# Kernel optimization log

Hardware: AMD Instinct MI355X
Metric: run time of the kernel (lower is better)

The kernel has to match this reference:

```python
import jax, jax.numpy as jnp
import numpy as np

N, NF, INF, NHID = 8192, 128, 128, 16


def _gcn(x, adj, dis, W, b):
    # GraphConvolution: support = x @ W; aggregate with distance-weighted adjacency
    support = x @ W  # [N, out]
    return (adj * dis) @ support + b


def setup_inputs() -> dict:
    key = jax.random.key(0)
    ks = jax.random.split(key, 26)

    def lin(k, i, o):
        kw, kb = jax.random.split(k)
        W = jax.random.uniform(kw, (i, o), jnp.float32, -1.0, 1.0) / np.sqrt(i).astype(np.float32)
        b = jax.random.uniform(kb, (o,), jnp.float32, -1.0, 1.0) / np.sqrt(i).astype(np.float32)
        return W, b

    x = jax.random.normal(ks[0], (N, NF), jnp.float32)
    adj = jax.random.uniform(ks[1], (N, N), jnp.float32)
    dis = jax.random.uniform(ks[2], (N, N), jnp.float32)

    W1, b1 = lin(ks[3], NF, NF)        # linear1
    Wg1, bg1 = lin(ks[4], NF, INF)     # gc1
    Wm1, bm1 = lin(ks[5], INF, 64)     # linear_med1
    Wm2, bm2 = lin(ks[6], 64, 128)     # linear_med2
    Wm3, bm3 = lin(ks[7], 128, 64)     # linear_med3
    Wm4, bm4 = lin(ks[8], 64, 64)      # linear_med4
    Wgh, bgh = lin(ks[9], 64, 64)      # gconv_hidden[0]
    W2, b2 = lin(ks[10], 64, 32)       # linear2
    Wg2, bg2 = lin(ks[11], 32, 32)     # gc2
    W3, b3 = lin(ks[12], 32, NHID)     # linear3

    return dict(x=x, adj=adj, dis=dis, W1=W1, b1=b1, Wg1=Wg1, bg1=bg1,
                Wm1=Wm1, bm1=bm1, Wm2=Wm2, bm2=bm2, Wm3=Wm3, bm3=bm3,
                Wm4=Wm4, bm4=bm4, Wgh=Wgh, bgh=bgh, W2=W2, b2=b2,
                Wg2=Wg2, bg2=bg2, W3=W3, b3=b3)


def reference(x, adj, dis, W1, b1, Wg1, bg1, Wm1, bm1, Wm2, bm2, Wm3, bm3,
              Wm4, bm4, Wgh, bgh, W2, b2, Wg2, bg2, W3, b3):
    lrelu = lambda v: jax.nn.leaky_relu(v, 0.2)
    x0 = _gcn(x @ W1 + b1, adj, dis, Wg1, bg1)
    x0 = lrelu(x0 @ Wm1 + bm1)
    x0 = lrelu(x0 @ Wm2 + bm2)
    x0 = lrelu(x0 @ Wm3 + bm3)
    x0 = jax.nn.relu(x0 @ Wm4 + bm4)
    x_res = x0
    x0 = jax.nn.relu(_gcn(x0, adj, dis, Wgh, bgh) + x_res)  # one hidden gconv layer
    x0 = x0 @ W2 + b2
    x0 = _gcn(x0, adj, dis, Wg2, bg2)
    return x0 @ W3 + b3
```

## Files before the change

kernel.cpp:

```cpp
#include <hip/hip_runtime.h>
#include <hip/hip_bf16.h>

#define NROWS 8192
typedef unsigned short u16;
typedef short bf16x8 __attribute__((ext_vector_type(8)));
typedef short bf16x4 __attribute__((ext_vector_type(4)));
typedef float f32x4 __attribute__((ext_vector_type(4)));

__device__ __forceinline__ u16 f2b(float f) {
    unsigned u = __float_as_uint(f);
    unsigned r = (u + 0x7fffu + ((u >> 16) & 1u)) >> 16;
    return (u16)r;
}
__device__ __forceinline__ float b2f(u16 v) {
    return __uint_as_float(((unsigned)v) << 16);
}

template<int MODE> __device__ __forceinline__ float actf(float v) {
    if constexpr (MODE == 1) return fmaxf(v, 0.f);
    else if constexpr (MODE == 2) return v > 0.f ? v : 0.2f * v;
    else return v;
}

__global__ __launch_bounds__(256) void fold1(
    const float* __restrict__ W1, const float* __restrict__ b1,
    const float* __restrict__ Wg1,
    const float* __restrict__ W2, const float* __restrict__ b2,
    const float* __restrict__ Wg2, float* __restrict__ ws) {
    float* T2 = ws + 9376;
    float* v1 = ws + 11424;
    float* v2 = ws + 11552;
    float* T1 = ws + 16384;
    const int tid = threadIdx.x, b = blockIdx.x;
    if (b < 16) {
        int i = b * 8 + (tid >> 5), j4 = (tid & 31) << 2;
        float4 acc = {0, 0, 0, 0};
        for (int k = 0; k < 128; ++k) {
            float a = W1[i * 128 + k];
            float4 g = *(const float4*)&Wg1[k * 128 + j4];
            acc.x += a * g.x; acc.y += a * g.y; acc.z += a * g.z; acc.w += a * g.w;
        }
        *(float4*)&T1[i * 128 + j4] = acc;
    } else if (b == 16) {
        if (tid < 128) {
            float s = 0;
            for (int k = 0; k < 128; ++k) s += b1[k] * Wg1[k * 128 + tid];
            v1[tid] = s;
        } else if (tid < 160) {
            int j = tid - 128;
            float s = 0;
            for (int k = 0; k < 32; ++k) s += b2[k] * Wg2[k * 32 + j];
            v2[j] = s;
        }
    } else {
        for (int o4 = tid; o4 < 64 * 8; o4 += 256) {
            int i = o4 >> 3, j4 = (o4 & 7) << 2;
            float4 acc = {0, 0, 0, 0};
            for (int k = 0; k < 32; ++k) {
                float a = W2[i * 32 + k];
                float4 g = *(const float4*)&Wg2[k * 32 + j4];
                acc.x += a * g.x; acc.y += a * g.y; acc.z += a * g.z; acc.w += a * g.w;
            }
            *(float4*)&T2[i * 32 + j4] = acc;
        }
    }
}

__global__ __launch_bounds__(256) void fold2(
    const float* __restrict__ Wm1, const float* __restrict__ bm1,
    const float* __restrict__ bg1,
    const float* __restrict__ W3, const float* __restrict__ b3,
    const float* __restrict__ bg2, float* __restrict__ ws) {
    float* WA = ws + 0;
    float* bA = ws + 8192;
    float* cA = ws + 8256;
    float* WB = ws + 8320;
    float* bB = ws + 9344;
    float* cB = ws + 9360;
    const float* T2 = ws + 9376;
    const float* v1 = ws + 11424;
    const float* v2 = ws + 11552;
    const float* T1 = ws + 16384;
    const int tid = threadIdx.x, b = blockIdx.x;
    if (b < 8) {
        int i = b * 16 + (tid >> 4), j4 = (tid & 15) << 2;
        float4 acc = {0, 0, 0, 0};
        for (int k = 0; k < 128; ++k) {
            float a = T1[i * 128 + k];
            float4 g = *(const float4*)&Wm1[k * 64 + j4];
            acc.x += a * g.x; acc.y += a * g.y; acc.z += a * g.z; acc.w += a * g.w;
        }
        *(float4*)&WA[i * 64 + j4] = acc;
    } else if (b == 8) {
        if (tid < 64) {
            float s = 0, c = 0;
            for (int k = 0; k < 128; ++k) {
                s += v1[k] * Wm1[k * 64 + tid];
                c += bg1[k] * Wm1[k * 64 + tid];
            }
            bA[tid] = s; cA[tid] = c + bm1[tid];
        } else if (tid < 80) {
            int j = tid - 64;
            float s = 0, c = 0;
            for (int k = 0; k < 32; ++k) {
                s += v2[k] * W3[k * 16 + j];
                c += bg2[k] * W3[k * 16 + j];
            }
            bB[j] = s; cB[j] = c + b3[j];
        }
    } else {
        int i = tid >> 2, j4 = (tid & 3) << 2;
        float4 acc = {0, 0, 0, 0};
        for (int k = 0; k < 32; ++k) {
            float a = T2[i * 32 + k];
            float4 g = *(const float4*)&W3[k * 16 + j4];
            acc.x += a * g.x; acc.y += a * g.y; acc.z += a * g.z; acc.w += a * g.w;
        }
        *(float4*)&WB[i * 16 + j4] = acc;
    }
}

template<int K, int M, int AIN, int AOUT, int OUTT>
__global__ __launch_bounds__(256) void gemm_rows(
    const float* __restrict__ in, const float* __restrict__ W,
    const float* __restrict__ bias, void* __restrict__ outv) {
    constexpr int RB = 32;
    constexpr int TNs = (M >= 64) ? 4 : 2;
    constexpr int TXs = M / TNs;
    constexpr int TYs = 256 / TXs;
    constexpr int TMs = RB / TYs;
    static_assert(TMs >= 1 && TMs * TYs == RB, "bad cfg");
    __shared__ float in_t[K][RB + 4];
    __shared__ float w_s[K * M];
    __shared__ float bias_s[M];
    const int tid = threadIdx.x;
    const int b0 = blockIdx.x * RB;
    constexpr int K4 = K / 4;
    for (int g = tid; g < RB * K4; g += 256) {
        int r = g / K4, c4 = g % K4;
        float4 v = *(const float4*)&in[(size_t)(b0 + r) * K + c4 * 4];
        v.x = actf<AIN>(v.x); v.y = actf<AIN>(v.y);
        v.z = actf<AIN>(v.z); v.w = actf<AIN>(v.w);
        in_t[c4 * 4 + 0][r] = v.x;
        in_t[c4 * 4 + 1][r] = v.y;
        in_t[c4 * 4 + 2][r] = v.z;
        in_t[c4 * 4 + 3][r] = v.w;
    }
    for (int g = tid; g < K * M / 4; g += 256)
        ((float4*)w_s)[g] = ((const float4*)W)[g];
    if (tid < M) bias_s[tid] = bias ? bias[tid] : 0.f;
    __syncthreads();

    const int tx = tid % TXs, ty = tid / TXs;
    const int c0 = tx * TNs, r0 = ty * TMs;
    float acc[TMs][TNs] = {};
    for (int k = 0; k < K; ++k) {
        float a[TMs];
#pragma unroll
        for (int m = 0; m < TMs; ++m) a[m] = in_t[k][r0 + m];
        float w[TNs];
#pragma unroll
        for (int n = 0; n < TNs; ++n) w[n] = w_s[k * M + c0 + n];
#pragma unroll
        for (int m = 0; m < TMs; ++m)
#pragma unroll
            for (int n = 0; n < TNs; ++n) acc[m][n] += a[m] * w[n];
    }
#pragma unroll
    for (int m = 0; m < TMs; ++m) {
        float vres[TNs];
#pragma unroll
        for (int n = 0; n < TNs; ++n) vres[n] = actf<AOUT>(acc[m][n] + bias_s[c0 + n]);
        if constexpr (OUTT == 0) {
            float* op = &((float*)outv)[(size_t)(b0 + r0 + m) * M + c0];
            if constexpr (TNs == 4) { float4 o4 = {vres[0], vres[1], vres[2], vres[3]}; *(float4*)op = o4; }
            else                    { float2 o2 = {vres[0], vres[1]}; *(float2*)op = o2; }
        } else {
            u16* ot = (u16*)outv;
#pragma unroll
            for (int n = 0; n < TNs; ++n)
                ot[(size_t)(c0 + n) * NROWS + (b0 + r0 + m)] = f2b(vres[n]);
        }
    }
}

template<int K, int M, int AOUT, int OMODE>
__device__ __forceinline__ void layer_step(
    const float (*pin)[17], const float* __restrict__ w,
    const float* __restrict__ bias,
    float (*pout)[17], float* __restrict__ gout, u16* __restrict__ stout,
    int b0, int tid) {
    constexpr int TXs = M / 4;
    constexpr int TYs = 256 / TXs;
    constexpr int TMs = 16 / TYs;
    static_assert(TMs >= 1, "cfg");
    const int tx = tid % TXs, ty = tid / TXs;
    const int c0 = tx * 4, r0 = ty * TMs;
    float acc[TMs][4] = {};
    for (int k = 0; k < K; ++k) {
        float4 wv = *(const float4*)&w[k * M + c0];
#pragma unroll
        for (int m = 0; m < TMs; ++m) {
            float a = pin[k][r0 + m];
            acc[m][0] += a * wv.x; acc[m][1] += a * wv.y;
            acc[m][2] += a * wv.z; acc[m][3] += a * wv.w;
        }
    }
#pragma unroll
    for (int m = 0; m < TMs; ++m) {
        float v[4];
#pragma unroll
        for (int n = 0; n < 4; ++n) {
            float bv = bias ? bias[c0 + n] : 0.f;
            v[n] = actf<AOUT>(acc[m][n] + bv);
        }
        if constexpr (OMODE != 2) {
#pragma unroll
            for (int n = 0; n < 4; ++n) pout[c0 + n][r0 + m] = v[n];
        }
        if constexpr (OMODE == 1) {
            float4 o = {v[0], v[1], v[2], v[3]};
            *(float4*)&gout[(size_t)(b0 + r0 + m) * M + c0] = o;
        }
        if constexpr (OMODE == 2) {
#pragma unroll
            for (int n = 0; n < 4; ++n)
                stout[(size_t)(c0 + n) * NROWS + (b0 + r0 + m)] = f2b(v[n]);
        }
    }
}

__global__ __launch_bounds__(256) void med_chain(
    const float* __restrict__ gA,
    const float* __restrict__ Wm2, const float* __restrict__ bm2,
    const float* __restrict__ Wm3, const float* __restrict__ bm3,
    const float* __restrict__ Wm4, const float* __restrict__ bm4,
    const float* __restrict__ Wgh,
    float* __restrict__ h4, u16* __restrict__ St) {
    __shared__ __align__(16) float P0[64][17];
    __shared__ __align__(16) float P1[128][17];
    __shared__ __align__(16) float P2[64][17];
    const int tid = threadIdx.x;
    const int b0 = blockIdx.x * 16;

    {
        int r = tid >> 4, c4 = tid & 15;
        float4 v = *(const float4*)&gA[(size_t)(b0 + r) * 64 + c4 * 4];
        P0[c4 * 4 + 0][r] = actf<2>(v.x);
        P0[c4 * 4 + 1][r] = actf<2>(v.y);
        P0[c4 * 4 + 2][r] = actf<2>(v.z);
        P0[c4 * 4 + 3][r] = actf<2>(v.w);
    }
    __syncthreads();
    layer_step<64, 128, 2, 0>(P0, Wm2, bm2, P1, nullptr, nullptr, b0, tid);
    __syncthreads();
    layer_step<128, 64, 2, 0>(P1, Wm3, bm3, P2, nullptr, nullptr, b0, tid);
    __syncthreads();
    layer_step<64, 64, 1, 1>(P2, Wm4, bm4, P0, h4, nullptr, b0, tid);
    __syncthreads();
    layer_step<64, 64, 0, 2>(P0, Wgh, nullptr, nullptr, nullptr, St, b0, tid);
}

#define LOAD_A(KC) \
    if constexpr (MODE == 0) { \
        _Pragma("unroll") for (int r = 0; r < AR8; ++r) { \
            int e8 = r * 256 + tid; \
            rA[r] = *(const bf16x8*)(Abf + (size_t)(i0 + (e8 >> 4)) * NROWS + (KC) + (e8 & 15) * 8); \
        } \
    } else { \
        _Pragma("unroll") for (int r = 0; r < AR4; ++r) { \
            int e4 = r * 256 + tid; \
            size_t g = (size_t)(i0 + (e4 >> 5)) * NROWS + (KC) + (e4 & 31) * 4; \
            rAa[r] = __builtin_nontemporal_load((const f32x4*)(adj + g)); \
            rAd[r] = __builtin_nontemporal_load((const f32x4*)(dis + g)); \
        } \
    }

#define LOAD_B(KC) \
    _Pragma("unroll") for (int r = 0; r < BR8; ++r) { \
        int e8 = r * 256 + tid; \
        rB[r] = *(const bf16x8*)(St + (size_t)(e8 >> 4) * NROWS + (KC) + (e8 & 15) * 8); \
    }

#define STORE_A(KC) \
    if constexpr (MODE == 0) { \
        _Pragma("unroll") for (int r = 0; r < AR8; ++r) { \
            int e8 = r * 256 + tid; int row = e8 >> 4; int col = (e8 & 15) * 8; \
            int bo = ((row * BK + col) * 2) ^ ((row & 7) << 4); \
            *(bf16x8*)((char*)As + bo) = rA[r]; \
        } \
    } else { \
        _Pragma("unroll") for (int r = 0; r < AR4; ++r) { \
            int e4 = r * 256 + tid; int row = e4 >> 5; int col = (e4 & 31) * 4; \
            bf16x4 v; \
            _Pragma("unroll") for (int j = 0; j < 4; ++j) v[j] = (short)f2b(rAa[r][j] * rAd[r][j]); \
            if constexpr (MODE == 1) \
                *(bf16x4*)(Abf + (size_t)(i0 + row) * NROWS + (KC) + col) = v; \
            int bo = ((row * BK + col) * 2) ^ ((row & 7) << 4); \
            *(bf16x4*)((char*)As + bo) = v; \
        } \
    }

#define STORE_B() \
    _Pragma("unroll") for (int r = 0; r < BR8; ++r) { \
        int e8 = r * 256 + tid; int c = e8 >> 4; int col = (e8 & 15) * 8; \
        int bo = ((c * BK + col) * 2) ^ ((c & 7) << 4); \
        *(bf16x8*)((char*)Bs + bo) = rB[r]; \
    }

template<int F, int MODE, int KS>
__global__ __launch_bounds__(256) void agg_mfma(
    u16* __restrict__ Abf, const float* __restrict__ adj,
    const float* __restrict__ dis, const u16* __restrict__ St,
    u16* __restrict__ Pout) {
    constexpr int CT = F / 16;
    constexpr int BK = 128;
    constexpr int KCH = NROWS / KS;
    constexpr int NCH = KCH / BK;
    constexpr int AR8 = (64 * BK) / (256 * 8);
    constexpr int AR4 = (64 * BK) / (256 * 4);
    constexpr int BR8 = (F * BK) / (256 * 8);
    __shared__ __align__(16) u16 As[64 * BK];
    __shared__ __align__(16) u16 Bs[F * BK];
    const int tid  = threadIdx.x;
    const int lane = tid & 63;
    const int wid  = tid >> 6;
    const int i0   = blockIdx.x * 64;
    const int ky   = blockIdx.y;
    const int l15  = lane & 15;
    const int kb   = (lane >> 4) * 8;
    const int k0   = ky * KCH;
    f32x4 acc[CT] = {};
    bf16x8 rA[AR8];
    f32x4 rAa[AR4], rAd[AR4];
    bf16x8 rB[BR8];

    LOAD_A(k0)
    LOAD_B(k0)
    for (int ch = 0; ch < NCH; ++ch) {
        const int kc = k0 + ch * BK;
        __syncthreads();
        STORE_A(kc)
        STORE_B()
        __syncthreads();
        if (ch + 1 < NCH) {
            LOAD_A(kc + BK)
            LOAD_B(kc + BK)
        }
#pragma unroll
        for (int ks = 0; ks < BK; ks += 32) {
            const int arow = wid * 16 + l15;
            int ao = ((arow * BK + ks + kb) * 2) ^ ((arow & 7) << 4);
            bf16x8 af = *(const bf16x8*)((const char*)As + ao);
#pragma unroll
            for (int ct = 0; ct < CT; ++ct) {
                int bcol = ct * 16 + l15;
                int bo = ((bcol * BK + ks + kb) * 2) ^ ((bcol & 7) << 4);
                bf16x8 bf = *(const bf16x8*)((const char*)Bs + bo);
                acc[ct] = __builtin_amdgcn_mfma_f32_16x16x32_bf16(af, bf, acc[ct], 0, 0, 0);
            }
        }
    }
    u16* P = Pout + (size_t)ky * ((size_t)NROWS * F);
    const int rb = i0 + wid * 16 + (lane >> 4) * 4;
#pragma unroll
    for (int ct = 0; ct < CT; ++ct)
#pragma unroll
        for (int i = 0; i < 4; ++i)
            P[(size_t)(rb + i) * F + ct * 16 + l15] = f2b(acc[ct][i]);
}
#undef LOAD_A
#undef LOAD_B
#undef STORE_A
#undef STORE_B

template<int F, int KS>
__global__ __launch_bounds__(256) void reduce_add(
    const u16* __restrict__ P, const float* __restrict__ bias,
    const float* __restrict__ res, float* __restrict__ out) {
    constexpr int TOT8 = NROWS * F / 8;
    int i8 = blockIdx.x * 256 + threadIdx.x;
    if (i8 >= TOT8) return;
    constexpr size_t STR = (size_t)NROWS * F;
    float s[8] = {};
#pragma unroll
    for (int k = 0; k < KS; ++k) {
        bf16x8 v = *(const bf16x8*)(P + (size_t)k * STR + (size_t)i8 * 8);
#pragma unroll
        for (int j = 0; j < 8; ++j) s[j] += b2f((u16)v[j]);
    }
    const int c0 = (i8 * 8) % F;
#pragma unroll
    for (int j = 0; j < 8; ++j) s[j] += bias[c0 + j];
    if (res) {
        const float4* r4 = (const float4*)(res + (size_t)i8 * 8);
        float4 ra = r4[0], rb = r4[1];
        s[0] += ra.x; s[1] += ra.y; s[2] += ra.z; s[3] += ra.w;
        s[4] += rb.x; s[5] += rb.y; s[6] += rb.z; s[7] += rb.w;
    }
    float4* o4 = (float4*)(out + (size_t)i8 * 8);
    float4 oa = {s[0], s[1], s[2], s[3]}, ob = {s[4], s[5], s[6], s[7]};
    o4[0] = oa; o4[1] = ob;
}

extern "C" void kernel_launch(void* const* d_in, const int* in_sizes, int n_in,
                              void* d_out, int out_size, void* d_ws, size_t ws_size,
                              hipStream_t stream) {
    const float* x   = (const float*)d_in[0];
    const float* adj = (const float*)d_in[1];
    const float* dis = (const float*)d_in[2];
    const float* W1  = (const float*)d_in[3];
    const float* b1  = (const float*)d_in[4];
    const float* Wg1 = (const float*)d_in[5];
    const float* bg1 = (const float*)d_in[6];
    const float* Wm1 = (const float*)d_in[7];
    const float* bm1 = (const float*)d_in[8];
    const float* Wm2 = (const float*)d_in[9];
    const float* bm2 = (const float*)d_in[10];
    const float* Wm3 = (const float*)d_in[11];
    const float* bm3 = (const float*)d_in[12];
    const float* Wm4 = (const float*)d_in[13];
    const float* bm4 = (const float*)d_in[14];
    const float* Wgh = (const float*)d_in[15];
    const float* bgh = (const float*)d_in[16];
    const float* W2  = (const float*)d_in[17];
    const float* b2  = (const float*)d_in[18];
    const float* Wg2 = (const float*)d_in[19];
    const float* bg2 = (const float*)d_in[20];
    const float* W3  = (const float*)d_in[21];
    const float* b3  = (const float*)d_in[22];
    float* ws  = (float*)d_ws;
    float* out = (float*)d_out;

    constexpr int KS = 8;
    const size_t ABF_FLOATS = (size_t)NROWS * NROWS / 2;
    const size_t P_FLOATS = (size_t)KS * NROWS * 64 / 2;
    const size_t BASE_FLOATS = 40960 + 262144 + P_FLOATS + 524288 + 524288;
    const size_t NEED_PRE_BYTES = (ABF_FLOATS + BASE_FLOATS) * 4ULL;
    const bool pre = ws_size >= NEED_PRE_BYTES;

    float* base = ws + (pre ? ABF_FLOATS : 0);
    float* wsW  = base;
    float* St_f = wsW + 40960;
    float* P_f  = St_f + 262144;
    float* gA   = P_f + P_FLOATS;
    float* h4   = gA + 524288;
    float* g2   = gA;

    u16* Abf = (u16*)ws;
    u16* St  = (u16*)St_f;
    u16* P   = (u16*)P_f;
    const float* WA = wsW + 0;
    const float* bA = wsW + 8192;
    const float* cA = wsW + 8256;
    const float* WB = wsW + 8320;
    const float* bB = wsW + 9344;
    const float* cB = wsW + 9360;

    fold1<<<18, 256, 0, stream>>>(W1, b1, Wg1, W2, b2, Wg2, wsW);
    fold2<<<10, 256, 0, stream>>>(Wm1, bm1, bg1, W3, b3, bg2, wsW);

    gemm_rows<128, 64, 0, 0, 1><<<256, 256, 0, stream>>>(x, WA, bA, St);
    if (pre) agg_mfma<64, 1, KS><<<dim3(128, KS), 256, 0, stream>>>(Abf, adj, dis, St, P);
    else     agg_mfma<64, 2, KS><<<dim3(128, KS), 256, 0, stream>>>(nullptr, adj, dis, St, P);
    reduce_add<64, KS><<<256, 256, 0, stream>>>(P, cA, nullptr, gA);

    med_chain<<<512, 256, 0, stream>>>(gA, Wm2, bm2, Wm3, bm3, Wm4, bm4, Wgh, h4, St);

    if (pre) agg_mfma<64, 0, KS><<<dim3(128, KS), 256, 0, stream>>>(Abf, nullptr, nullptr, St, P);
    else     agg_mfma<64, 2, KS><<<dim3(128, KS), 256, 0, stream>>>(nullptr, adj, dis, St, P);
    reduce_add<64, KS><<<256, 256, 0, stream>>>(P, bgh, h4, g2);

    gemm_rows<64, 16, 1, 0, 1><<<256, 256, 0, stream>>>(g2, WB, bB, St);
    if (pre) agg_mfma<16, 0, KS><<<dim3(128, KS), 256, 0, stream>>>(Abf, nullptr, nullptr, St, P);
    else     agg_mfma<16, 2, KS><<<dim3(128, KS), 256, 0, stream>>>(nullptr, adj, dis, St, P);
    reduce_add<16, KS><<<64, 256, 0, stream>>>(P, cB, nullptr, out);
}
```

Before: 312.8 us.

## Fuse split-K partial reductions into consumers and double-buffer the bf16 aggregation path

The split-K partial-sum reduction for the first two aggregations moves into the kernels that consume it: med_chain sums the partials plus bias before its layers, and a new gemm_sB sums partials, adds the residual, applies relu and runs the 64->16 projection. This removes two reduce_add launches and the fp32 intermediate round trips. The precomputed-bf16 (MODE 0) aggregation path now uses two register sets, so loads run two chunks ahead of the MFMA phase to hide more global latency, at the cost of higher register pressure. gemm_rows is specialised into a fixed gemm_sA.

```diff
diff --git a/kernel.cpp b/kernel.cpp
--- a/kernel.cpp
+++ b/kernel.cpp
@@ -120,27 +120,18 @@
     }
 }
 
-template<int K, int M, int AIN, int AOUT, int OUTT>
-__global__ __launch_bounds__(256) void gemm_rows(
+__global__ __launch_bounds__(256) void gemm_sA(
     const float* __restrict__ in, const float* __restrict__ W,
-    const float* __restrict__ bias, void* __restrict__ outv) {
-    constexpr int RB = 32;
-    constexpr int TNs = (M >= 64) ? 4 : 2;
-    constexpr int TXs = M / TNs;
-    constexpr int TYs = 256 / TXs;
-    constexpr int TMs = RB / TYs;
-    static_assert(TMs >= 1 && TMs * TYs == RB, "bad cfg");
+    const float* __restrict__ bias, u16* __restrict__ St) {
+    constexpr int K = 128, M = 64, RB = 32;
     __shared__ float in_t[K][RB + 4];
     __shared__ float w_s[K * M];
     __shared__ float bias_s[M];
     const int tid = threadIdx.x;
     const int b0 = blockIdx.x * RB;
-    constexpr int K4 = K / 4;
-    for (int g = tid; g < RB * K4; g += 256) {
-        int r = g / K4, c4 = g % K4;
+    for (int g = tid; g < RB * (K / 4); g += 256) {
+        int r = g / (K / 4), c4 = g % (K / 4);
         float4 v = *(const float4*)&in[(size_t)(b0 + r) * K + c4 * 4];
-        v.x = actf<AIN>(v.x); v.y = actf<AIN>(v.y);
-        v.z = actf<AIN>(v.z); v.w = actf<AIN>(v.w);
         in_t[c4 * 4 + 0][r] = v.x;
         in_t[c4 * 4 + 1][r] = v.y;
         in_t[c4 * 4 + 2][r] = v.z;
@@ -148,40 +139,23 @@
     }
     for (int g = tid; g < K * M / 4; g += 256)
         ((float4*)w_s)[g] = ((const float4*)W)[g];
-    if (tid < M) bias_s[tid] = bias ? bias[tid] : 0.f;
+    if (tid < M) bias_s[tid] = bias[tid];
     __syncthreads();
 
-    const int tx = tid % TXs, ty = tid / TXs;
-    const int c0 = tx * TNs, r0 = ty * TMs;
-    float acc[TMs][TNs] = {};
+    const int tx = tid & 15, ty = tid >> 4;
+    const int c0 = tx * 4, r0 = ty * 2;
+    float acc[2][4] = {};
     for (int k = 0; k < K; ++k) {
-        float a[TMs];
-#pragma unroll
-        for (int m = 0; m < TMs; ++m) a[m] = in_t[k][r0 + m];
-        float w[TNs];
-#pragma unroll
-        for (int n = 0; n < TNs; ++n) w[n] = w_s[k * M + c0 + n];
-#pragma unroll
-        for (int m = 0; m < TMs; ++m)
-#pragma unroll
-            for (int n = 0; n < TNs; ++n) acc[m][n] += a[m] * w[n];
-    }
-#pragma unroll
-    for (int m = 0; m < TMs; ++m) {
-        float vres[TNs];
-#pragma unroll
-        for (int n = 0; n < TNs; ++n) vres[n] = actf<AOUT>(acc[m][n] + bias_s[c0 + n]);
-        if constexpr (OUTT == 0) {
-            float* op = &((float*)outv)[(size_t)(b0 + r0 + m) * M + c0];
-            if constexpr (TNs == 4) { float4 o4 = {vres[0], vres[1], vres[2], vres[3]}; *(float4*)op = o4; }
-            else                    { float2 o2 = {vres[0], vres[1]}; *(float2*)op = o2; }
-        } else {
-            u16* ot = (u16*)outv;
-#pragma unroll
-            for (int n = 0; n < TNs; ++n)
-                ot[(size_t)(c0 + n) * NROWS + (b0 + r0 + m)] = f2b(vres[n]);
-        }
-    }
+        float a0 = in_t[k][r0], a1 = in_t[k][r0 + 1];
+        float4 wv = *(const float4*)&w_s[k * M + c0];
+        acc[0][0] += a0 * wv.x; acc[0][1] += a0 * wv.y; acc[0][2] += a0 * wv.z; acc[0][3] += a0 * wv.w;
+        acc[1][0] += a1 * wv.x; acc[1][1] += a1 * wv.y; acc[1][2] += a1 * wv.z; acc[1][3] += a1 * wv.w;
+    }
+#pragma unroll
+    for (int m = 0; m < 2; ++m)
+#pragma unroll
+        for (int n = 0; n < 4; ++n)
+            St[(size_t)(c0 + n) * NROWS + (b0 + r0 + m)] = f2b(acc[m][n] + bias_s[c0 + n]);
 }
 
 template<int K, int M, int AOUT, int OMODE>
@@ -230,8 +204,9 @@
     }
 }
 
+template<int KS>
 __global__ __launch_bounds__(256) void med_chain(
-    const float* __restrict__ gA,
+    const u16* __restrict__ P, const float* __restrict__ cA,
     const float* __restrict__ Wm2, const float* __restrict__ bm2,
     const float* __restrict__ Wm3, const float* __restrict__ bm3,
     const float* __restrict__ Wm4, const float* __restrict__ bm4,
@@ -242,14 +217,21 @@
     __shared__ __align__(16) float P2[64][17];
     const int tid = threadIdx.x;
     const int b0 = blockIdx.x * 16;
+    constexpr size_t STR = (size_t)NROWS * 64;
 
     {
-        int r = tid >> 4, c4 = tid & 15;
-        float4 v = *(const float4*)&gA[(size_t)(b0 + r) * 64 + c4 * 4];
-        P0[c4 * 4 + 0][r] = actf<2>(v.x);
-        P0[c4 * 4 + 1][r] = actf<2>(v.y);
-        P0[c4 * 4 + 2][r] = actf<2>(v.z);
-        P0[c4 * 4 + 3][r] = actf<2>(v.w);
+        int r = tid >> 4, c4 = (tid & 15) * 4;
+        float s[4];
+        float4 cv = *(const float4*)&cA[c4];
+        s[0] = cv.x; s[1] = cv.y; s[2] = cv.z; s[3] = cv.w;
+#pragma unroll
+        for (int k = 0; k < KS; ++k) {
+            bf16x4 v = *(const bf16x4*)(P + (size_t)k * STR + (size_t)(b0 + r) * 64 + c4);
+#pragma unroll
+            for (int j = 0; j < 4; ++j) s[j] += b2f((u16)v[j]);
+        }
+#pragma unroll
+        for (int j = 0; j < 4; ++j) P0[c4 + j][r] = actf<2>(s[j]);
     }
     __syncthreads();
     layer_step<64, 128, 2, 0>(P0, Wm2, bm2, P1, nullptr, nullptr, b0, tid);
@@ -261,51 +243,110 @@
     layer_step<64, 64, 0, 2>(P0, Wgh, nullptr, nullptr, nullptr, St, b0, tid);
 }
 
-#define LOAD_A(KC) \
-    if constexpr (MODE == 0) { \
-        _Pragma("unroll") for (int r = 0; r < AR8; ++r) { \
-            int e8 = r * 256 + tid; \
-            rA[r] = *(const bf16x8*)(Abf + (size_t)(i0 + (e8 >> 4)) * NROWS + (KC) + (e8 & 15) * 8); \
-        } \
-    } else { \
-        _Pragma("unroll") for (int r = 0; r < AR4; ++r) { \
-            int e4 = r * 256 + tid; \
-            size_t g = (size_t)(i0 + (e4 >> 5)) * NROWS + (KC) + (e4 & 31) * 4; \
-            rAa[r] = __builtin_nontemporal_load((const f32x4*)(adj + g)); \
-            rAd[r] = __builtin_nontemporal_load((const f32x4*)(dis + g)); \
-        } \
-    }
-
-#define LOAD_B(KC) \
+template<int KS>
+__global__ __launch_bounds__(256) void gemm_sB(
+    const u16* __restrict__ P, const float* __restrict__ bgh,
+    const float* __restrict__ h4,
+    const float* __restrict__ WB, const float* __restrict__ bB,
+    u16* __restrict__ St) {
+    constexpr int K = 64, M = 16, RB = 32;
+    __shared__ float in_t[K][RB + 4];
+    __shared__ float w_s[K * M];
+    const int tid = threadIdx.x;
+    const int b0 = blockIdx.x * RB;
+    constexpr size_t STR = (size_t)NROWS * 64;
+
+    for (int g = tid; g < RB * 16; g += 256) {
+        int r = g >> 4, c4 = (g & 15) * 4;
+        float s[4];
+        float4 bv = *(const float4*)&bgh[c4];
+        s[0] = bv.x; s[1] = bv.y; s[2] = bv.z; s[3] = bv.w;
+#pragma unroll
+        for (int k = 0; k < KS; ++k) {
+            bf16x4 v = *(const bf16x4*)(P + (size_t)k * STR + (size_t)(b0 + r) * 64 + c4);
+#pragma unroll
+            for (int j = 0; j < 4; ++j) s[j] += b2f((u16)v[j]);
+        }
+        float4 hv = *(const float4*)&h4[(size_t)(b0 + r) * 64 + c4];
+        in_t[c4 + 0][r] = fmaxf(s[0] + hv.x, 0.f);
+        in_t[c4 + 1][r] = fmaxf(s[1] + hv.y, 0.f);
+        in_t[c4 + 2][r] = fmaxf(s[2] + hv.z, 0.f);
+        in_t[c4 + 3][r] = fmaxf(s[3] + hv.w, 0.f);
+    }
+    for (int g = tid; g < K * M / 4; g += 256)
+        ((float4*)w_s)[g] = ((const float4*)WB)[g];
+    __syncthreads();
+
+    const int tx = tid & 7, ty = tid >> 3;
+    const int c0 = tx * 2, r0 = ty;
+    float a0 = 0, a1 = 0;
+    for (int k = 0; k < K; ++k) {
+        float a = in_t[k][r0];
+        a0 += a * w_s[k * M + c0];
+        a1 += a * w_s[k * M + c0 + 1];
+    }
+    St[(size_t)(c0 + 0) * NROWS + (b0 + r0)] = f2b(a0 + bB[c0]);
+    St[(size_t)(c0 + 1) * NROWS + (b0 + r0)] = f2b(a1 + bB[c0 + 1]);
+}
+
+#define LOADA_F(KC) \
+    _Pragma("unroll") for (int r = 0; r < AR4; ++r) { \
+        int e4 = r * 256 + tid; \
+        size_t g = (size_t)(i0 + (e4 >> 5)) * NROWS + (KC) + (e4 & 31) * 4; \
+        rAa[r] = __builtin_nontemporal_load((const f32x4*)(adj + g)); \
+        rAd[r] = __builtin_nontemporal_load((const f32x4*)(dis + g)); \
+    }
+
+#define STOREA_F(KC) \
+    _Pragma("unroll") for (int r = 0; r < AR4; ++r) { \
+        int e4 = r * 256 + tid; int row = e4 >> 5; int col = (e4 & 31) * 4; \
+        bf16x4 v; \
+        _Pragma("unroll") for (int j = 0; j < 4; ++j) v[j] = (short)f2b(rAa[r][j] * rAd[r][j]); \
+        if constexpr (MODE == 1) \
+            *(bf16x4*)(Abf + (size_t)(i0 + row) * NROWS + (KC) + col) = v; \
+        int bo = ((row * BK + col) * 2) ^ ((row & 7) << 4); \
+        *(bf16x4*)((char*)As + bo) = v; \
+    }
+
+#define LOADA_S(S, KC) \
+    _Pragma("unroll") for (int r = 0; r < AR8; ++r) { \
+        int e8 = r * 256 + tid; \
+        rA##S[r] = *(const bf16x8*)(Abf + (size_t)(i0 + (e8 >> 4)) * NROWS + (KC) + (e8 & 15) * 8); \
+    }
+
+#define STOREA_S(S) \
+    _Pragma("unroll") for (int r = 0; r < AR8; ++r) { \
+        int e8 = r * 256 + tid; int row = e8 >> 4; int col = (e8 & 15) * 8; \
+        int bo = ((row * BK + col) * 2) ^ ((row & 7) << 4); \
+        *(bf16x8*)((char*)As + bo) = rA##S[r]; \
+    }
+
+#define LOADB_S(S, KC) \
     _Pragma("unroll") for (int r = 0; r < BR8; ++r) { \
         int e8 = r * 256 + tid; \
-        rB[r] = *(const bf16x8*)(St + (size_t)(e8 >> 4) * NROWS + (KC) + (e8 & 15) * 8); \
-    }
-
-#define STORE_A(KC) \
-    if constexpr (MODE == 0) { \
-        _Pragma("unroll") for (int r = 0; r < AR8; ++r) { \
-            int e8 = r * 256 + tid; int row = e8 >> 4; int col = (e8 & 15) * 8; \
-            int bo = ((row * BK + col) * 2) ^ ((row & 7) << 4); \
-            *(bf16x8*)((char*)As + bo) = rA[r]; \
-        } \
-    } else { \
-        _Pragma("unroll") for (int r = 0; r < AR4; ++r) { \
-            int e4 = r * 256 + tid; int row = e4 >> 5; int col = (e4 & 31) * 4; \
-            bf16x4 v; \
-            _Pragma("unroll") for (int j = 0; j < 4; ++j) v[j] = (short)f2b(rAa[r][j] * rAd[r][j]); \
-            if constexpr (MODE == 1) \
-                *(bf16x4*)(Abf + (size_t)(i0 + row) * NROWS + (KC) + col) = v; \
-            int bo = ((row * BK + col) * 2) ^ ((row & 7) << 4); \
-            *(bf16x4*)((char*)As + bo) = v; \
-        } \
-    }
-
-#define STORE_B() \
+        rB##S[r] = *(const bf16x8*)(St + (size_t)(e8 >> 4) * NROWS + (KC) + (e8 & 15) * 8); \
+    }
+
+#define STOREB_S(S) \
     _Pragma("unroll") for (int r = 0; r < BR8; ++r) { \
         int e8 = r * 256 + tid; int c = e8 >> 4; int col = (e8 & 15) * 8; \
         int bo = ((c * BK + col) * 2) ^ ((c & 7) << 4); \
-        *(bf16x8*)((char*)Bs + bo) = rB[r]; \
+        *(bf16x8*)((char*)Bs + bo) = rB##S[r]; \
+    }
+
+#define MFMA_PHASE() \
+    _Pragma("unroll") \
+    for (int ks = 0; ks < BK; ks += 32) { \
+        const int arow = wid * 16 + l15; \
+        int ao = ((arow * BK + ks + kb) * 2) ^ ((arow & 7) << 4); \
+        bf16x8 af = *(const bf16x8*)((const char*)As + ao); \
+        _Pragma("unroll") \
+        for (int ct = 0; ct < CT; ++ct) { \
+            int bcol = ct * 16 + l15; \
+            int bo = ((bcol * BK + ks + kb) * 2) ^ ((bcol & 7) << 4); \
+            bf16x8 bf = *(const bf16x8*)((const char*)Bs + bo); \
+            acc[ct] = __builtin_amdgcn_mfma_f32_16x16x32_bf16(af, bf, acc[ct], 0, 0, 0); \
+        } \
     }
 
 template<int F, int MODE, int KS>
@@ -317,6 +358,7 @@
     constexpr int BK = 128;
     constexpr int KCH = NROWS / KS;
     constexpr int NCH = KCH / BK;
+    static_assert((NCH & 1) == 0, "even NCH");
     constexpr int AR8 = (64 * BK) / (256 * 8);
     constexpr int AR4 = (64 * BK) / (256 * 4);
     constexpr int BR8 = (F * BK) / (256 * 8);
@@ -331,34 +373,38 @@
     const int kb   = (lane >> 4) * 8;
     const int k0   = ky * KCH;
     f32x4 acc[CT] = {};
-    bf16x8 rA[AR8];
-    f32x4 rAa[AR4], rAd[AR4];
-    bf16x8 rB[BR8];
-
-    LOAD_A(k0)
-    LOAD_B(k0)
-    for (int ch = 0; ch < NCH; ++ch) {
-        const int kc = k0 + ch * BK;
-        __syncthreads();
-        STORE_A(kc)
-        STORE_B()
-        __syncthreads();
-        if (ch + 1 < NCH) {
-            LOAD_A(kc + BK)
-            LOAD_B(kc + BK)
-        }
-#pragma unroll
-        for (int ks = 0; ks < BK; ks += 32) {
-            const int arow = wid * 16 + l15;
-            int ao = ((arow * BK + ks + kb) * 2) ^ ((arow & 7) << 4);
-            bf16x8 af = *(const bf16x8*)((const char*)As + ao);
-#pragma unroll
-            for (int ct = 0; ct < CT; ++ct) {
-                int bcol = ct * 16 + l15;
-                int bo = ((bcol * BK + ks + kb) * 2) ^ ((bcol & 7) << 4);
-                bf16x8 bf = *(const bf16x8*)((const char*)Bs + bo);
-                acc[ct] = __builtin_amdgcn_mfma_f32_16x16x32_bf16(af, bf, acc[ct], 0, 0, 0);
-            }
+
+    if constexpr (MODE == 0) {
+        bf16x8 rAX[AR8], rAY[AR8];
+        bf16x8 rBX[BR8], rBY[BR8];
+        LOADA_S(X, k0) LOADB_S(X, k0)
+        LOADA_S(Y, k0 + BK) LOADB_S(Y, k0 + BK)
+        for (int ch = 0; ch < NCH; ch += 2) {
+            const int kc = k0 + ch * BK;
+            __syncthreads();
+            STOREA_S(X) STOREB_S(X)
+            __syncthreads();
+            if (ch + 2 < NCH) { LOADA_S(X, kc + 2 * BK) LOADB_S(X, kc + 2 * BK) }
+            MFMA_PHASE()
+            __syncthreads();
+            STOREA_S(Y) STOREB_S(Y)
+            __syncthreads();
+            if (ch + 3 < NCH) { LOADA_S(Y, kc + 3 * BK) LOADB_S(Y, kc + 3 * BK) }
+            MFMA_PHASE()
+        }
+    } else {
+        f32x4 rAa[AR4], rAd[AR4];
+        bf16x8 rBX[BR8];
+        LOADA_F(k0)
+        LOADB_S(X, k0)
+        for (int ch = 0; ch < NCH; ++ch) {
+            const int kc = k0 + ch * BK;
+            __syncthreads();
+            STOREA_F(kc)
+            STOREB_S(X)
+            __syncthreads();
+            if (ch + 1 < NCH) { LOADA_F(kc + BK) LOADB_S(X, kc + BK) }
+            MFMA_PHASE()
         }
     }
     u16* P = Pout + (size_t)ky * ((size_t)NROWS * F);
@@ -369,15 +415,18 @@
         for (int i = 0; i < 4; ++i)
             P[(size_t)(rb + i) * F + ct * 16 + l15] = f2b(acc[ct][i]);
 }
-#undef LOAD_A
-#undef LOAD_B
-#undef STORE_A
-#undef STORE_B
+#undef LOADA_F
+#undef STOREA_F
+#undef LOADA_S
+#undef STOREA_S
+#undef LOADB_S
+#undef STOREB_S
+#undef MFMA_PHASE
 
 template<int F, int KS>
 __global__ __launch_bounds__(256) void reduce_add(
     const u16* __restrict__ P, const float* __restrict__ bias,
-    const float* __restrict__ res, float* __restrict__ out) {
+    float* __restrict__ out) {
     constexpr int TOT8 = NROWS * F / 8;
     int i8 = blockIdx.x * 256 + threadIdx.x;
     if (i8 >= TOT8) return;
@@ -392,12 +441,6 @@
     const int c0 = (i8 * 8) % F;
 #pragma unroll
     for (int j = 0; j < 8; ++j) s[j] += bias[c0 + j];
-    if (res) {
-        const float4* r4 = (const float4*)(res + (size_t)i8 * 8);
-        float4 ra = r4[0], rb = r4[1];
-        s[0] += ra.x; s[1] += ra.y; s[2] += ra.z; s[3] += ra.w;
-        s[4] += rb.x; s[5] += rb.y; s[6] += rb.z; s[7] += rb.w;
-    }
     float4* o4 = (float4*)(out + (size_t)i8 * 8);
     float4 oa = {s[0], s[1], s[2], s[3]}, ob = {s[4], s[5], s[6], s[7]};
     o4[0] = oa; o4[1] = ob;
@@ -435,7 +478,7 @@
     constexpr int KS = 8;
     const size_t ABF_FLOATS = (size_t)NROWS * NROWS / 2;
     const size_t P_FLOATS = (size_t)KS * NROWS * 64 / 2;
-    const size_t BASE_FLOATS = 40960 + 262144 + P_FLOATS + 524288 + 524288;
+    const size_t BASE_FLOATS = 40960 + 262144 + P_FLOATS + 524288;
     const size_t NEED_PRE_BYTES = (ABF_FLOATS + BASE_FLOATS) * 4ULL;
     const bool pre = ws_size >= NEED_PRE_BYTES;
 
@@ -443,9 +486,7 @@
     float* wsW  = base;
     float* St_f = wsW + 40960;
     float* P_f  = St_f + 262144;
-    float* gA   = P_f + P_FLOATS;
-    float* h4   = gA + 524288;
-    float* g2   = gA;
+    float* h4   = P_f + P_FLOATS;
 
     u16* Abf = (u16*)ws;
     u16* St  = (u16*)St_f;
@@ -460,19 +501,18 @@
     fold1<<<18, 256, 0, stream>>>(W1, b1, Wg1, W2, b2, Wg2, wsW);
     fold2<<<10, 256, 0, stream>>>(Wm1, bm1, bg1, W3, b3, bg2, wsW);
 
-    gemm_rows<128, 64, 0, 0, 1><<<256, 256, 0, stream>>>(x, WA, bA, St);
+    gemm_sA<<<256, 256, 0, stream>>>(x, WA, bA, St);
     if (pre) agg_mfma<64, 1, KS><<<dim3(128, KS), 256, 0, stream>>>(Abf, adj, dis, St, P);
     else     agg_mfma<64, 2, KS><<<dim3(128, KS), 256, 0, stream>>>(nullptr, adj, dis, St, P);
-    reduce_add<64, KS><<<256, 256, 0, stream>>>(P, cA, nullptr, gA);
-
-    med_chain<<<512, 256, 0, stream>>>(gA, Wm2, bm2, Wm3, bm3, Wm4, bm4, Wgh, h4, St);
+
+    med_chain<KS><<<512, 256, 0, stream>>>(P, cA, Wm2, bm2, Wm3, bm3, Wm4, bm4, Wgh, h4, St);
 
     if (pre) agg_mfma<64, 0, KS><<<dim3(128, KS), 256, 0, stream>>>(Abf, nullptr, nullptr, St, P);
     else     agg_mfma<64, 2, KS><<<dim3(128, KS), 256, 0, stream>>>(nullptr, adj, dis, St, P);
-    reduce_add<64, KS><<<256, 256, 0, stream>>>(P, bgh, h4, g2);
-
-    gemm_rows<64, 16, 1, 0, 1><<<256, 256, 0, stream>>>(g2, WB, bB, St);
+
+    gemm_sB<KS><<<256, 256, 0, stream>>>(P, bgh, h4, WB, bB, St);
+
     if (pre) agg_mfma<16, 0, KS><<<dim3(128, KS), 256, 0, stream>>>(Abf, nullptr, nullptr, St, P);
     else     agg_mfma<16, 2, KS><<<dim3(128, KS), 256, 0, stream>>>(nullptr, adj, dis, St, P);
-    reduce_add<16, KS><<<64, 256, 0, stream>>>(P, cB, nullptr, out);
-}
+    reduce_add<16, KS><<<64, 256, 0, stream>>>(P, cB, out);
+}
```

After: 321.1 us. +2.6%, slower.
